# Kernel tuning notes

Measured on AMD Instinct MI355X. Metric: run time of the kernel, lower is better.

The kernel has to match this reference:

```python
import jax, jax.numpy as jnp
import numpy as np

D_MODEL = 1024
N_HEADS = 16
LN_EPS = 1e-6  # flax LayerNorm default

def setup_inputs() -> dict:
    key = jax.random.key(0)
    k1, k2, k3 = jax.random.split(key, 3)
    B, S = 2, 2048
    x = jax.random.normal(k1, (B, S, D_MODEL), dtype=jnp.float32)
    W_qkv = jax.random.normal(k2, (D_MODEL, 3 * D_MODEL), dtype=jnp.float32) / np.sqrt(D_MODEL)
    W_out = jax.random.normal(k3, (D_MODEL, D_MODEL), dtype=jnp.float32) / np.sqrt(D_MODEL)
    q_scale = jnp.ones((D_MODEL,), dtype=jnp.float32)
    k_scale = jnp.ones((D_MODEL,), dtype=jnp.float32)
    return {"x": x, "W_qkv": W_qkv, "q_scale": q_scale, "k_scale": k_scale, "W_out": W_out}

def _layernorm(t, scale):
    mu = jnp.mean(t, axis=-1, keepdims=True)
    var = jnp.var(t, axis=-1, keepdims=True)
    return (t - mu) * jax.lax.rsqrt(var + LN_EPS) * scale

def reference(x, W_qkv, q_scale, k_scale, W_out):
    B, S, D = x.shape
    H = N_HEADS
    Hd = D // H
    # fused QKV projection (no bias)
    qkv = jnp.einsum('bsd,de->bse', x, W_qkv)
    q, k, v = jnp.split(qkv, 3, axis=-1)
    # QK-LayerNorm over full d_model (before head split), scale only
    q = _layernorm(q, q_scale)
    k = _layernorm(k, k_scale)
    # split heads: [b, s, h, hd]
    q = q.reshape(B, S, H, Hd)
    k = k.reshape(B, S, H, Hd)
    v = v.reshape(B, S, H, Hd)
    # eager attention with causal mask
    scores = jnp.einsum('bshd,bthd->bhst', q / jnp.sqrt(Hd).astype(q.dtype), k)  # [b,h,s,t]
    future = jnp.triu(jnp.ones((S, S), dtype=bool), 1)  # True on strictly-future positions
    scores = jnp.where(future[None, None, :, :], jnp.finfo(scores.dtype).min, scores)
    attn = jax.nn.softmax(scores, axis=-1)
    ctx = jnp.einsum('bhst,bthd->bshd', attn, v)
    out = jnp.einsum('bsd,de->bse', ctx.reshape(B, S, D), W_out)
    return out
```

## Files before the change

kernel.cpp:

```cpp
#include <hip/hip_runtime.h>
#include <cstdint>
#include <cstddef>

typedef __attribute__((ext_vector_type(8))) short short8;
typedef __attribute__((ext_vector_type(4))) float floatx4;

__device__ __forceinline__ float bf2f(unsigned short u) {
  union { unsigned int i; float f; } c; c.i = ((unsigned int)u) << 16; return c.f;
}
__device__ __forceinline__ unsigned short f2bf(float f) {
  union { float f; unsigned int i; } c; c.f = f;
  unsigned int r = c.i + 0x7fffu + ((c.i >> 16) & 1u);
  return (unsigned short)(r >> 16);
}
__device__ __forceinline__ unsigned int fbits(float f) {
  union { float f; unsigned int i; } c; c.f = f; return c.i;
}

__device__ __forceinline__ void glds16(const unsigned short* g, unsigned short* l) {
  __builtin_amdgcn_global_load_lds((const __attribute__((address_space(1))) void*)g,
                                   (__attribute__((address_space(3))) void*)l, 16, 0, 0);
}

__device__ __forceinline__ void tr_tile(const float* __restrict__ in,
                                        unsigned short* __restrict__ out,
                                        int R, int C, int bx, int by, int tid,
                                        unsigned short (*t)[33]) {
  const int cx = tid & 31, rl = tid >> 5;
#pragma unroll
  for (int i = 0; i < 4; ++i)
    t[rl + i * 8][cx] = f2bf(in[(size_t)(by * 32 + rl + i * 8) * C + bx * 32 + cx]);
  __syncthreads();
  const int oc = by * 32 + cx;
#pragma unroll
  for (int i = 0; i < 4; ++i)
    out[(size_t)(bx * 32 + rl + i * 8) * R + oc] = t[cx][rl + i * 8];
}

__global__ __launch_bounds__(256) void k_prep(const float* __restrict__ x,
                                              const float* __restrict__ Wq,
                                              const float* __restrict__ Wo,
                                              unsigned short* __restrict__ x_bf,
                                              unsigned short* __restrict__ WTq,
                                              unsigned short* __restrict__ WTo) {
  __shared__ unsigned short t[32][33];
  const int bid = blockIdx.x, tid = threadIdx.x;
  if (bid < 3072) {
    tr_tile(Wq, WTq, 1024, 3072, bid % 96, bid / 96, tid, t);
  } else if (bid < 4096) {
    int v = bid - 3072;
    tr_tile(Wo, WTo, 1024, 1024, v & 31, v >> 5, tid, t);
  } else {
    int i = (bid - 4096) * 256 + tid;
    float4 v = ((const float4*)x)[i];
    ushort4 o = { f2bf(v.x), f2bf(v.y), f2bf(v.z), f2bf(v.w) };
    ((ushort4*)x_bf)[i] = o;
  }
}

template <int MT, bool F32OUT>
__global__ __launch_bounds__(256) void k_gemm_bt(const unsigned short* __restrict__ A,
                                                 const unsigned short* __restrict__ BT,
                                                 void* __restrict__ Cout,
                                                 int M, int N, int K) {
  constexpr int NI = MT / 32;
  __shared__ unsigned short As[2][MT * 32];
  __shared__ unsigned short Bs[2][128 * 32];
  const int bm = blockIdx.x * MT, bn = blockIdx.y * 128;
  const int tid = threadIdx.x;
  const int wave = tid >> 6, lane = tid & 63;
  const int wm = (wave & 1) * (MT / 2), wn = (wave >> 1) * 64;
  const int lrow = lane & 15, lgrp = lane >> 4;
  floatx4 acc[NI][4] = {};

  const int lr4 = lane >> 2, lc8 = (lane & 3) * 8;
  const int br0 = wave * 32;
  const unsigned short* Bg0 = BT + (size_t)(bn + br0 + lr4) * K + lc8;
  const unsigned short* Bg1 = BT + (size_t)(bn + br0 + 16 + lr4) * K + lc8;
  const int ar0 = wave * (MT / 4);
  const unsigned short* Ag0 = A + (size_t)(bm + ar0 + lr4) * K + lc8;
  const unsigned short* Ag1 = A + (size_t)(bm + ar0 + 16 + lr4) * K + lc8;

  for (int k0 = 0; k0 < K; k0 += 64) {
#pragma unroll
    for (int u = 0; u < 2; ++u) {
      const int ko = k0 + u * 32;
      glds16(Ag0 + ko, &As[u][ar0 * 32]);
      if (MT == 128) glds16(Ag1 + ko, &As[u][(ar0 + 16) * 32]);
      glds16(Bg0 + ko, &Bs[u][br0 * 32]);
      glds16(Bg1 + ko, &Bs[u][(br0 + 16) * 32]);
    }
    __syncthreads();
#pragma unroll
    for (int u = 0; u < 2; ++u) {
      short8 a[NI], bfr[4];
#pragma unroll
      for (int i = 0; i < NI; ++i)
        a[i] = *(const short8*)&As[u][(wm + i * 16 + lrow) * 32 + lgrp * 8];
#pragma unroll
      for (int j = 0; j < 4; ++j)
        bfr[j] = *(const short8*)&Bs[u][(wn + j * 16 + lrow) * 32 + lgrp * 8];
#pragma unroll
      for (int i = 0; i < NI; ++i)
#pragma unroll
        for (int j = 0; j < 4; ++j)
          acc[i][j] = __builtin_amdgcn_mfma_f32_16x16x32_bf16(a[i], bfr[j], acc[i][j], 0, 0, 0);
    }
    __syncthreads();
  }
#pragma unroll
  for (int i = 0; i < NI; ++i)
#pragma unroll
    for (int j = 0; j < 4; ++j)
#pragma unroll
      for (int r = 0; r < 4; ++r) {
        int m = bm + wm + i * 16 + lgrp * 4 + r;
        int n = bn + wn + j * 16 + lrow;
        if (F32OUT)
          ((float*)Cout)[(size_t)m * N + n] = acc[i][j][r];
        else
          ((unsigned short*)Cout)[(size_t)m * N + n] = f2bf(acc[i][j][r]);
      }
}

__global__ __launch_bounds__(256) void k_lnv(const unsigned short* __restrict__ qkv,
                                             const float* __restrict__ q_scale,
                                             const float* __restrict__ k_scale,
                                             unsigned short* __restrict__ q_n,
                                             unsigned short* __restrict__ k_n,
                                             unsigned short* __restrict__ VT) {
  const int bid = blockIdx.x, tid = threadIdx.x;
  if (bid < 4096) {
    const int tok = bid;
    const int wave = tid >> 6, lane = tid & 63;
    __shared__ float red[2][4];
    const unsigned short* row = qkv + (size_t)tok * 3072;
#pragma unroll
    for (int seg = 0; seg < 2; ++seg) {
      const unsigned short* p  = row + seg * 1024;
      const float* sc = seg ? k_scale : q_scale;
      unsigned short* outp = (seg ? k_n : q_n) + (size_t)tok * 1024;
      ushort4 u = *(const ushort4*)&p[tid * 4];
      float xv[4] = { bf2f(u.x), bf2f(u.y), bf2f(u.z), bf2f(u.w) };
      float sum = xv[0] + xv[1] + xv[2] + xv[3];
      float sq  = xv[0]*xv[0] + xv[1]*xv[1] + xv[2]*xv[2] + xv[3]*xv[3];
      for (int off = 32; off; off >>= 1) {
        sum += __shfl_down(sum, off, 64);
        sq  += __shfl_down(sq,  off, 64);
      }
      if (lane == 0) { red[0][wave] = sum; red[1][wave] = sq; }
      __syncthreads();
      sum = red[0][0] + red[0][1] + red[0][2] + red[0][3];
      sq  = red[1][0] + red[1][1] + red[1][2] + red[1][3];
      __syncthreads();
      float mean = sum * (1.0f / 1024.0f);
      float var  = sq * (1.0f / 1024.0f) - mean * mean;
      float rstd = rsqrtf(var + 1e-6f);
      if (seg == 0) rstd *= 0.18033688011112042f;
      float4 su = *(const float4*)&sc[tid * 4];
      ushort4 o;
      o.x = f2bf((xv[0] - mean) * rstd * su.x);
      o.y = f2bf((xv[1] - mean) * rstd * su.y);
      o.z = f2bf((xv[2] - mean) * rstd * su.z);
      o.w = f2bf((xv[3] - mean) * rstd * su.w);
      *(ushort4*)&outp[tid * 4] = o;
    }
  } else {
    __shared__ unsigned short t[32][33];
    const int v = bid - 4096;
    const int bh = v & 31, b = bh >> 4, h = bh & 15;
    const int sy = (v >> 5) & 63, hx = v >> 11;
    const int cx = tid & 31, rl = tid >> 5;
#pragma unroll
    for (int i = 0; i < 4; ++i)
      t[rl + i * 8][cx] =
        qkv[(size_t)(b * 2048 + sy * 32 + rl + i * 8) * 3072 + 2048 + h * 64 + hx * 32 + cx];
    __syncthreads();
#pragma unroll
    for (int i = 0; i < 4; ++i)
      VT[((size_t)bh * 64 + hx * 32 + rl + i * 8) * 2048 + sy * 32 + cx] = t[cx][rl + i * 8];
  }
}


#define KS_STRIDE 72
#define VS_STRIDE 72
#define PS_STRIDE 72

#define MFMA_BF16 __builtin_amdgcn_mfma_f32_16x16x32_bf16

template <bool MASKED>
__device__ __forceinline__ void attn_step(int t0, int q0, int wq, int wt,
    const short8 (&qa)[2][2],
    const unsigned short* Ks, const unsigned short* Vs, unsigned short* Psq,
    floatx4 (&o)[2][4], floatx4 (&o_l)[2], int lrow, int lgrp) {
  const int twbase = wt * 32;
#pragma unroll
  for (int tb = 0; tb < 2; ++tb) {
    short8 kb0 = *(const short8*)&Ks[(twbase + tb * 16 + lrow) * KS_STRIDE + lgrp * 8];
    short8 kb1 = *(const short8*)&Ks[(twbase + tb * 16 + lrow) * KS_STRIDE + 32 + lgrp * 8];
#pragma unroll
    for (int qb = 0; qb < 2; ++qb) {
      floatx4 st = {};
      st = MFMA_BF16(kb0, qa[qb][0], st, 0, 0, 0);
      st = MFMA_BF16(kb1, qa[qb][1], st, 0, 0, 0);
      float p0 = exp2f(st[0]), p1 = exp2f(st[1]);
      float p2 = exp2f(st[2]), p3 = exp2f(st[3]);
      if (MASKED) {
        const int qcol = q0 + wq * 32 + qb * 16 + lrow;
        const int tbase = t0 + twbase + tb * 16 + lgrp * 4;
        p0 = (tbase     <= qcol) ? p0 : 0.0f;
        p1 = (tbase + 1 <= qcol) ? p1 : 0.0f;
        p2 = (tbase + 2 <= qcol) ? p2 : 0.0f;
        p3 = (tbase + 3 <= qcol) ? p3 : 0.0f;
      }
      uint2 pu;
      pu.x = __builtin_amdgcn_perm(fbits(p1), fbits(p0), 0x07060302u);
      pu.y = __builtin_amdgcn_perm(fbits(p3), fbits(p2), 0x07060302u);
      *(uint2*)&Psq[(qb * 16 + lrow) * PS_STRIDE + twbase + tb * 16 + lgrp * 4] = pu;
    }
  }
  const short8 vones = { 0x3F80, 0x3F80, 0x3F80, 0x3F80,
                         0x3F80, 0x3F80, 0x3F80, 0x3F80 };
  short8 pa0 = *(const short8*)&Psq[lrow * PS_STRIDE + twbase + lgrp * 8];
  short8 pa1 = *(const short8*)&Psq[(16 + lrow) * PS_STRIDE + twbase + lgrp * 8];
  o_l[0] = MFMA_BF16(pa0, vones, o_l[0], 0, 0, 0);
  o_l[1] = MFMA_BF16(pa1, vones, o_l[1], 0, 0, 0);
#pragma unroll
  for (int hb = 0; hb < 4; ++hb) {
    short8 vb = *(const short8*)&Vs[(hb * 16 + lrow) * VS_STRIDE + twbase + lgrp * 8];
    o[0][hb] = MFMA_BF16(pa0, vb, o[0][hb], 0, 0, 0);
    o[1][hb] = MFMA_BF16(pa1, vb, o[1][hb], 0, 0, 0);
  }
}

__global__ __launch_bounds__(256) void k_flash(const unsigned short* __restrict__ q_n,
                                               const unsigned short* __restrict__ k_n,
                                               const unsigned short* __restrict__ VT,
                                               unsigned short* __restrict__ ctx) {
  const int S = 2048, D = 1024;
  const int bh = blockIdx.x, b = bh >> 4, h = bh & 15;
  const int byi = (int)blockIdx.y, bi = byi & 7, bj = byi >> 3;
  const int qt = 8 * bj + ((bj & 1) ? (7 - bi) : bi);
  const int q0 = qt * 64;
  const int tid = threadIdx.x, wave = tid >> 6, lane = tid & 63;
  const int wq = wave >> 1, wt = wave & 1;
  const int lrow = lane & 15, lgrp = lane >> 4;

  __shared__ __align__(16) unsigned char smem[27648];
  unsigned short* Ks  = (unsigned short*)smem;
  unsigned short* Vs  = (unsigned short*)(smem + 9216);
  unsigned short* Psq = (unsigned short*)(smem + 18432) + wq * 32 * PS_STRIDE;
  float* buf  = (float*)smem;
  float* Lbuf = (float*)(smem + 17408);

  const unsigned short* kg = k_n + (size_t)(b * S) * D + h * 64;
  const unsigned short* vg = VT + (size_t)bh * 64 * S;
  const int sr = tid >> 3, sc = (tid & 7) * 8;

  short8 qa[2][2];
#pragma unroll
  for (int qb = 0; qb < 2; ++qb) {
    const unsigned short* qp =
        q_n + (size_t)(b * S + q0 + wq * 32 + qb * 16 + lrow) * D + h * 64;
    qa[qb][0] = *(const short8*)(qp + lgrp * 8);
    qa[qb][1] = *(const short8*)(qp + 32 + lgrp * 8);
  }
  floatx4 o[2][4] = {};
  floatx4 o_l[2] = {};

  const int tend = q0 + 64;
  for (int t0 = 0; t0 < tend; t0 += 64) {
    *(int4*)&Ks[sr * KS_STRIDE + sc]        = *(const int4*)(kg + (size_t)(t0 + sr) * D + sc);
    *(int4*)&Ks[(sr + 32) * KS_STRIDE + sc] = *(const int4*)(kg + (size_t)(t0 + sr + 32) * D + sc);
    *(int4*)&Vs[sr * VS_STRIDE + sc]        = *(const int4*)(vg + (size_t)sr * S + t0 + sc);
    *(int4*)&Vs[(sr + 32) * VS_STRIDE + sc] = *(const int4*)(vg + (size_t)(sr + 32) * S + t0 + sc);
    __syncthreads();
    if (t0 + 64 <= q0)
      attn_step<false>(t0, q0, wq, wt, qa, Ks, Vs, Psq, o, o_l, lrow, lgrp);
    else
      attn_step<true>(t0, q0, wq, wt, qa, Ks, Vs, Psq, o, o_l, lrow, lgrp);
    __syncthreads();
  }

  if (wt == 1) {
    if (lrow == 0) {
#pragma unroll
      for (int qb = 0; qb < 2; ++qb)
#pragma unroll
        for (int r = 0; r < 4; ++r)
          Lbuf[wq * 32 + qb * 16 + lgrp * 4 + r] = o_l[qb][r];
    }
    float* bf = buf + wq * 32 * 68;
#pragma unroll
    for (int qb = 0; qb < 2; ++qb)
#pragma unroll
      for (int hb = 0; hb < 4; ++hb)
#pragma unroll
        for (int r = 0; r < 4; ++r)
          bf[(qb * 16 + lgrp * 4 + r) * 68 + hb * 16 + lrow] = o[qb][hb][r];
  }
  __syncthreads();
  if (wt == 0) {
    float* bf = buf + wq * 32 * 68;
#pragma unroll
    for (int qb = 0; qb < 2; ++qb)
#pragma unroll
      for (int hb = 0; hb < 4; ++hb)
#pragma unroll
        for (int r = 0; r < 4; ++r)
          o[qb][hb][r] += bf[(qb * 16 + lgrp * 4 + r) * 68 + hb * 16 + lrow];
    unsigned short* op = ctx + (size_t)(b * S + q0 + wq * 32) * D + h * 64;
#pragma unroll
    for (int qb = 0; qb < 2; ++qb)
#pragma unroll
      for (int r = 0; r < 4; ++r) {
        float inv = 1.0f / (o_l[qb][r] + Lbuf[wq * 32 + qb * 16 + lgrp * 4 + r]);
        int row = qb * 16 + lgrp * 4 + r;
#pragma unroll
        for (int hb = 0; hb < 4; ++hb)
          op[(size_t)row * D + hb * 16 + lrow] = f2bf(o[qb][hb][r] * inv);
      }
  }
}

extern "C" void kernel_launch(void* const* d_in, const int* in_sizes, int n_in,
                              void* d_out, int out_size, void* d_ws, size_t ws_size,
                              hipStream_t stream) {
  const float* x       = (const float*)d_in[0];
  const float* W_qkv   = (const float*)d_in[1];
  const float* q_scale = (const float*)d_in[2];
  const float* k_scale = (const float*)d_in[3];
  const float* W_out   = (const float*)d_in[4];
  float* out = (float*)d_out;
  char* ws = (char*)d_ws;
  unsigned short* WT_qkv = (unsigned short*)(ws + 0);
  unsigned short* WT_out = (unsigned short*)(ws + 6291456);
  unsigned short* qkv    = (unsigned short*)(ws + 8388608);
  unsigned short* q_nb   = (unsigned short*)(ws + 33554432);
  unsigned short* k_nb   = (unsigned short*)(ws + 41943040);
  unsigned short* VT     = (unsigned short*)(ws + 50331648);
  unsigned short* x_bf   = (unsigned short*)(ws + 58720256);
  unsigned short* ctx    = qkv;

  k_prep<<<8192, 256, 0, stream>>>(x, W_qkv, W_out, x_bf, WT_qkv, WT_out);
  k_gemm_bt<128, false><<<dim3(32, 24), 256, 0, stream>>>(x_bf, WT_qkv, qkv, 4096, 3072, 1024);
  k_lnv<<<8192, 256, 0, stream>>>(qkv, q_scale, k_scale, q_nb, k_nb, VT);
  k_flash<<<dim3(32, 32), 256, 0, stream>>>(q_nb, k_nb, VT, ctx);
  k_gemm_bt<64, true><<<dim3(64, 8), 256, 0, stream>>>(ctx, WT_out, out, 4096, 1024, 1024);
}
```

Measured before the change: 194.6 us.

## Double-buffer K/V tiles via async global-to-LDS loads with XOR swizzle

The flash-attention kernel now stages K and V tiles directly into LDS with global_load_lds into two ping-pong buffers, so the next tile's loads overlap the current tile's MFMA work, and one barrier per iteration is dropped. Padded LDS strides are replaced by an XOR-swizzled 64-wide layout for K, V and P to avoid bank conflicts without padding. Query tiles are now scheduled longest-first instead of the old zigzag order. LDS use grows to 40 KB, which may reduce occupancy, and the loop relies on the async loads completing before the barrier.

```diff
diff --git a/kernel.cpp b/kernel.cpp
--- a/kernel.cpp
+++ b/kernel.cpp
@@ -183,10 +183,6 @@
 }
 
 
-#define KS_STRIDE 72
-#define VS_STRIDE 72
-#define PS_STRIDE 72
-
 #define MFMA_BF16 __builtin_amdgcn_mfma_f32_16x16x32_bf16
 
 template <bool MASKED>
@@ -195,10 +191,12 @@
     const unsigned short* Ks, const unsigned short* Vs, unsigned short* Psq,
     floatx4 (&o)[2][4], floatx4 (&o_l)[2], int lrow, int lgrp) {
   const int twbase = wt * 32;
+  const int sw = lrow & 7;
 #pragma unroll
   for (int tb = 0; tb < 2; ++tb) {
-    short8 kb0 = *(const short8*)&Ks[(twbase + tb * 16 + lrow) * KS_STRIDE + lgrp * 8];
-    short8 kb1 = *(const short8*)&Ks[(twbase + tb * 16 + lrow) * KS_STRIDE + 32 + lgrp * 8];
+    const int R = twbase + tb * 16 + lrow;
+    short8 kb0 = *(const short8*)&Ks[R * 64 + ((lgrp ^ sw) * 8)];
+    short8 kb1 = *(const short8*)&Ks[R * 64 + (((lgrp + 4) ^ sw) * 8)];
 #pragma unroll
     for (int qb = 0; qb < 2; ++qb) {
       floatx4 st = {};
@@ -217,18 +215,20 @@
       uint2 pu;
       pu.x = __builtin_amdgcn_perm(fbits(p1), fbits(p0), 0x07060302u);
       pu.y = __builtin_amdgcn_perm(fbits(p3), fbits(p2), 0x07060302u);
-      *(uint2*)&Psq[(qb * 16 + lrow) * PS_STRIDE + twbase + tb * 16 + lgrp * 4] = pu;
+      const int Bb = wt * 4 + tb * 2 + (lgrp >> 1);
+      *(uint2*)&Psq[(qb * 16 + lrow) * 64 + ((Bb ^ sw) * 8) + (lgrp & 1) * 4] = pu;
     }
   }
   const short8 vones = { 0x3F80, 0x3F80, 0x3F80, 0x3F80,
                          0x3F80, 0x3F80, 0x3F80, 0x3F80 };
-  short8 pa0 = *(const short8*)&Psq[lrow * PS_STRIDE + twbase + lgrp * 8];
-  short8 pa1 = *(const short8*)&Psq[(16 + lrow) * PS_STRIDE + twbase + lgrp * 8];
+  const int pblk = (wt * 4 + lgrp) ^ sw;
+  short8 pa0 = *(const short8*)&Psq[lrow * 64 + pblk * 8];
+  short8 pa1 = *(const short8*)&Psq[(16 + lrow) * 64 + pblk * 8];
   o_l[0] = MFMA_BF16(pa0, vones, o_l[0], 0, 0, 0);
   o_l[1] = MFMA_BF16(pa1, vones, o_l[1], 0, 0, 0);
 #pragma unroll
   for (int hb = 0; hb < 4; ++hb) {
-    short8 vb = *(const short8*)&Vs[(hb * 16 + lrow) * VS_STRIDE + twbase + lgrp * 8];
+    short8 vb = *(const short8*)&Vs[(hb * 16 + lrow) * 64 + pblk * 8];
     o[0][hb] = MFMA_BF16(pa0, vb, o[0][hb], 0, 0, 0);
     o[1][hb] = MFMA_BF16(pa1, vb, o[1][hb], 0, 0, 0);
   }
@@ -240,23 +240,39 @@
                                                unsigned short* __restrict__ ctx) {
   const int S = 2048, D = 1024;
   const int bh = blockIdx.x, b = bh >> 4, h = bh & 15;
-  const int byi = (int)blockIdx.y, bi = byi & 7, bj = byi >> 3;
-  const int qt = 8 * bj + ((bj & 1) ? (7 - bi) : bi);
+  const int qt = 31 - (int)blockIdx.y;
   const int q0 = qt * 64;
   const int tid = threadIdx.x, wave = tid >> 6, lane = tid & 63;
   const int wq = wave >> 1, wt = wave & 1;
   const int lrow = lane & 15, lgrp = lane >> 4;
 
-  __shared__ __align__(16) unsigned char smem[27648];
-  unsigned short* Ks  = (unsigned short*)smem;
-  unsigned short* Vs  = (unsigned short*)(smem + 9216);
-  unsigned short* Psq = (unsigned short*)(smem + 18432) + wq * 32 * PS_STRIDE;
+  __shared__ __align__(16) unsigned char smem[40960];
+  unsigned short* Ks0 = (unsigned short*)smem;
+  unsigned short* Ks1 = (unsigned short*)(smem + 8192);
+  unsigned short* Vs0 = (unsigned short*)(smem + 16384);
+  unsigned short* Vs1 = (unsigned short*)(smem + 24576);
+  unsigned short* Psq = (unsigned short*)(smem + 32768) + wq * 32 * 64;
   float* buf  = (float*)smem;
   float* Lbuf = (float*)(smem + 17408);
 
   const unsigned short* kg = k_n + (size_t)(b * S) * D + h * 64;
   const unsigned short* vg = VT + (size_t)bh * 64 * S;
-  const int sr = tid >> 3, sc = (tid & 7) * 8;
+
+  const int r0 = wave * 8 + (lane >> 3);
+  const int sblk = (lane & 7) ^ (r0 & 7);
+  const unsigned short* kst0 = kg + (size_t)r0 * D + sblk * 8;
+  const unsigned short* kst1 = kg + (size_t)(r0 + 32) * D + sblk * 8;
+  const unsigned short* vst0 = vg + (size_t)r0 * S + sblk * 8;
+  const unsigned short* vst1 = vg + (size_t)(r0 + 32) * S + sblk * 8;
+  const int ldso0 = wave * 512;
+  const int ldso1 = 2048 + wave * 512;
+
+#define STAGE(tn, Ksb, Vsb) do {                       \
+    glds16(kst0 + (size_t)(tn) * D, (Ksb) + ldso0);    \
+    glds16(kst1 + (size_t)(tn) * D, (Ksb) + ldso1);    \
+    glds16(vst0 + (tn),             (Vsb) + ldso0);    \
+    glds16(vst1 + (tn),             (Vsb) + ldso1);    \
+  } while (0)
 
   short8 qa[2][2];
 #pragma unroll
@@ -269,19 +285,23 @@
   floatx4 o[2][4] = {};
   floatx4 o_l[2] = {};
 
+  STAGE(0, Ks0, Vs0);
+  __syncthreads();
+
   const int tend = q0 + 64;
   for (int t0 = 0; t0 < tend; t0 += 64) {
-    *(int4*)&Ks[sr * KS_STRIDE + sc]        = *(const int4*)(kg + (size_t)(t0 + sr) * D + sc);
-    *(int4*)&Ks[(sr + 32) * KS_STRIDE + sc] = *(const int4*)(kg + (size_t)(t0 + sr + 32) * D + sc);
-    *(int4*)&Vs[sr * VS_STRIDE + sc]        = *(const int4*)(vg + (size_t)sr * S + t0 + sc);
-    *(int4*)&Vs[(sr + 32) * VS_STRIDE + sc] = *(const int4*)(vg + (size_t)(sr + 32) * S + t0 + sc);
+    const bool odd = (t0 >> 6) & 1;
+    unsigned short* Ksc = odd ? Ks1 : Ks0;
+    unsigned short* Vsc = odd ? Vs1 : Vs0;
+    if (t0 + 64 < tend)
+      STAGE(t0 + 64, odd ? Ks0 : Ks1, odd ? Vs0 : Vs1);
+    if (t0 + 64 <= q0)
+      attn_step<false>(t0, q0, wq, wt, qa, Ksc, Vsc, Psq, o, o_l, lrow, lgrp);
+    else
+      attn_step<true>(t0, q0, wq, wt, qa, Ksc, Vsc, Psq, o, o_l, lrow, lgrp);
     __syncthreads();
-    if (t0 + 64 <= q0)
-      attn_step<false>(t0, q0, wq, wt, qa, Ks, Vs, Psq, o, o_l, lrow, lgrp);
-    else
-      attn_step<true>(t0, q0, wq, wt, qa, Ks, Vs, Psq, o, o_l, lrow, lgrp);
-    __syncthreads();
-  }
+  }
+#undef STAGE
 
   if (wt == 1) {
     if (lrow == 0) {
```

New measurement: 185.5 us. -4.7%, faster.
